# Performance work log

Measured on AMD Instinct MI355X. Metric: run time of the kernel, lower is better.

The kernel has to match this reference:

```python
import jax, jax.numpy as jnp
import numpy as np

D_MODEL = 1024
NUM_HEADS = 16
HEAD_DIM = D_MODEL // NUM_HEADS
BATCH, SEQ = 4, 4096


def setup_inputs() -> dict:
    key = jax.random.key(0)
    ks = jax.random.split(key, 12)
    std = 0.02
    inp = {
        "query": jax.random.normal(ks[0], (BATCH, SEQ, D_MODEL), dtype=jnp.float32),
        "key": jax.random.normal(ks[1], (BATCH, SEQ, D_MODEL), dtype=jnp.float32),
        "value": jax.random.normal(ks[2], (BATCH, SEQ, D_MODEL), dtype=jnp.float32),
        "mask": jax.random.randint(ks[3], (BATCH, SEQ, 1, 1), 0, 2, dtype=jnp.int32),
        "Wq": jax.random.normal(ks[4], (D_MODEL, D_MODEL), dtype=jnp.float32) * std,
        "bq": jnp.zeros((D_MODEL,), dtype=jnp.float32),
        "Wk": jax.random.normal(ks[5], (D_MODEL, D_MODEL), dtype=jnp.float32) * std,
        "bk": jnp.zeros((D_MODEL,), dtype=jnp.float32),
        "Wv": jax.random.normal(ks[6], (D_MODEL, D_MODEL), dtype=jnp.float32) * std,
        "bv": jnp.zeros((D_MODEL,), dtype=jnp.float32),
        "Wo": jax.random.normal(ks[7], (D_MODEL, D_MODEL), dtype=jnp.float32) * std,
        "bo": jnp.zeros((D_MODEL,), dtype=jnp.float32),
    }
    return inp


def reference(query, key, value, mask, Wq, bq, Wk, bk, Wv, bv, Wo, bo):
    b = query.shape[0]
    # QKV projections (torch nn.Linear: x @ W.T + b)
    Q = query @ Wq.T + bq
    K = key @ Wk.T + bk
    V = value @ Wv.T + bv
    # [b, s, H, hd] -> [b, H, s, hd]
    Q = Q.reshape(b, -1, NUM_HEADS, HEAD_DIM).transpose(0, 2, 1, 3)
    K = K.reshape(b, -1, NUM_HEADS, HEAD_DIM).transpose(0, 2, 1, 3)
    V = V.reshape(b, -1, NUM_HEADS, HEAD_DIM).transpose(0, 2, 1, 3)
    # NOTE: faithful to the original's mislabeled einsum: tensors are [b,H,s,hd]
    # but labels treat axis1 as 'q' and axis2 as 'h', so energy is
    # [batch, seq, heads_q, heads_k] and softmax mixes over heads.
    energy = jnp.einsum('nqhd,nkhd->nhqk', Q, K)
    energy = jnp.where(mask == 0, jnp.float32(-1e20), energy)
    attention = jax.nn.softmax(energy / jnp.sqrt(jnp.float32(D_MODEL)), axis=3)
    # output labeled nqhd -> [b, heads, seq, hd]
    x = jnp.einsum('nhql,nlhd->nqhd', attention, V)
    x = x.transpose(0, 2, 1, 3).reshape(b, -1, D_MODEL)  # [b, s, d_model]
    return x @ Wo.T + bo
```

## Files before the change

kernel.cpp:

```cpp
#include <hip/hip_runtime.h>


typedef unsigned int u32;
typedef unsigned short u16;
typedef __attribute__((ext_vector_type(4))) float f32x4;
typedef __attribute__((ext_vector_type(8))) short bf16x8;

__device__ __forceinline__ void async_copy16(const void* g, void* l) {
  __builtin_amdgcn_global_load_lds(
      (const __attribute__((address_space(1))) void*)g,
      (__attribute__((address_space(3))) void*)l, 16, 0, 0);
}

__device__ __forceinline__ u32 pk_bf16(float a, float b) {
  u32 ua = (__builtin_bit_cast(u32, a) + 0x8000u) >> 16;
  u32 ub = (__builtin_bit_cast(u32, b) + 0x8000u) & 0xFFFF0000u;
  return ua | ub;
}
__device__ __forceinline__ float bflo(u32 u) { return __builtin_bit_cast(float, u << 16); }
__device__ __forceinline__ float bfhi(u32 u) { return __builtin_bit_cast(float, u & 0xFFFF0000u); }

struct F8 { float f[8]; };
__device__ __forceinline__ F8 unp8(uint4 u) {
  F8 r;
  r.f[0] = bflo(u.x); r.f[1] = bfhi(u.x);
  r.f[2] = bflo(u.y); r.f[3] = bfhi(u.y);
  r.f[4] = bflo(u.z); r.f[5] = bfhi(u.z);
  r.f[6] = bflo(u.w); r.f[7] = bfhi(u.w);
  return r;
}

__global__ void cvt_w4(const float* __restrict__ s0, const float* __restrict__ s1,
                       const float* __restrict__ s2, const float* __restrict__ s3,
                       u16* __restrict__ dst) {
  int z = blockIdx.y;
  const float* s = (z == 0) ? s0 : (z == 1) ? s1 : (z == 2) ? s2 : s3;
  u16* d = dst + (size_t)z * (1024 * 1024);
  int i = (blockIdx.x * 256 + threadIdx.x) * 4;
  float4 f = *(const float4*)(s + i);
  uint2 u;
  u.x = pk_bf16(f.x, f.y);
  u.y = pk_bf16(f.z, f.w);
  *(uint2*)(d + i) = u;
}

__global__ void cvt_in3(const float* __restrict__ s0, const float* __restrict__ s1,
                        const float* __restrict__ s2, u16* __restrict__ dst) {
  int z = blockIdx.y;
  const float* s = (z == 0) ? s0 : (z == 1) ? s1 : s2;
  u16* d = dst + (size_t)z * 16777216;
  int i = (blockIdx.x * 256 + threadIdx.x) * 4;
  float4 f = *(const float4*)(s + i);
  uint2 u;
  u.x = pk_bf16(f.x, f.y);
  u.y = pk_bf16(f.z, f.w);
  *(uint2*)(d + i) = u;
}

template <bool AF32, bool OUTBF>
__device__ __forceinline__ void gemm_tile(const void* __restrict__ Ap,
                                          const u16* __restrict__ Bp,
                                          const float* __restrict__ bias,
                                          void* __restrict__ Cp,
                                          int m0, int n0, u16* As, u16* Bs) {
  constexpr int KD = 1024;
  constexpr int ND = 1024;
  const int t = threadIdx.x;
  const int lane = t & 63, w = t >> 6;
  const int wr = (w >> 1) * 64, wc = (w & 1) * 64;
  const int lr = lane & 15, quad = lane >> 4;
  f32x4 acc[4][4] = {};

  for (int k0 = 0; k0 < KD; k0 += 32) {
    __syncthreads();
#pragma unroll
    for (int i = 0; i < 2; i++) {
      int c = i * 256 + t;
      int r = c >> 2, c8 = (c & 3) * 8;
      async_copy16(Bp + ((size_t)(n0 + r) * KD + k0 + c8), &Bs[c * 8]);
    }
    if constexpr (AF32) {
      const float* Af = (const float*)Ap;
      const int r = t >> 2, c8 = (t & 3) * 8;
      const float4* s0 = (const float4*)(Af + (size_t)(m0 + r) * KD + k0 + c8);
      const float4* s1 = (const float4*)(Af + (size_t)(m0 + 64 + r) * KD + k0 + c8);
      float4 f0 = s0[0], f1 = s0[1];
      float4 f2 = s1[0], f3 = s1[1];
      uint4 u0 = { pk_bf16(f0.x, f0.y), pk_bf16(f0.z, f0.w),
                   pk_bf16(f1.x, f1.y), pk_bf16(f1.z, f1.w) };
      uint4 u1 = { pk_bf16(f2.x, f2.y), pk_bf16(f2.z, f2.w),
                   pk_bf16(f3.x, f3.y), pk_bf16(f3.z, f3.w) };
      *(uint4*)&As[t * 8] = u0;
      *(uint4*)&As[(256 + t) * 8] = u1;
    } else {
      const u16* Ab = (const u16*)Ap;
#pragma unroll
      for (int i = 0; i < 2; i++) {
        int c = i * 256 + t;
        int r = c >> 2, c8 = (c & 3) * 8;
        async_copy16(Ab + ((size_t)(m0 + r) * KD + k0 + c8), &As[c * 8]);
      }
    }
    __syncthreads();

    bf16x8 af[4], bfr[4];
#pragma unroll
    for (int mi = 0; mi < 4; mi++)
      af[mi] = *(const bf16x8*)&As[(wr + mi * 16 + lr) * 32 + quad * 8];
#pragma unroll
    for (int ni = 0; ni < 4; ni++)
      bfr[ni] = *(const bf16x8*)&Bs[(wc + ni * 16 + lr) * 32 + quad * 8];
#pragma unroll
    for (int mi = 0; mi < 4; mi++)
#pragma unroll
      for (int ni = 0; ni < 4; ni++)
        acc[mi][ni] = __builtin_amdgcn_mfma_f32_16x16x32_bf16(af[mi], bfr[ni], acc[mi][ni], 0, 0, 0);
  }

#pragma unroll
  for (int ni = 0; ni < 4; ni++) {
    int col = n0 + wc + ni * 16 + lr;
    float bv = bias[col];
#pragma unroll
    for (int mi = 0; mi < 4; mi++) {
      int row = m0 + wr + mi * 16 + quad * 4;
#pragma unroll
      for (int r = 0; r < 4; r++) {
        float val = acc[mi][ni][r] + bv;
        if constexpr (OUTBF) {
          ((u16*)Cp)[(size_t)(row + r) * ND + col] =
              (u16)((__builtin_bit_cast(u32, val) + 0x8000u) >> 16);
        } else {
          ((float*)Cp)[(size_t)(row + r) * ND + col] = val;
        }
      }
    }
  }
}

template <bool AF32>
__global__ __launch_bounds__(256) void gemm_qkv(
    const void* __restrict__ a0, const void* __restrict__ a1, const void* __restrict__ a2,
    const u16* __restrict__ W, const float* __restrict__ b0, const float* __restrict__ b1,
    const float* __restrict__ b2, u16* __restrict__ out) {
  __shared__ alignas(16) u16 As[128 * 32];
  __shared__ alignas(16) u16 Bs[128 * 32];
  const int lin = blockIdx.x;
  const int c = lin & 7;
  const int i = lin >> 3;
  const int z = i >> 7;
  const int r = i & 127;
  const int m = c * 16 + (r >> 3);
  const int n = r & 7;
  const void* A = (z == 0) ? a0 : (z == 1) ? a1 : a2;
  const float* bias = (z == 0) ? b0 : (z == 1) ? b1 : b2;
  gemm_tile<AF32, true>(A, W + (size_t)z * 1048576, bias, out + (size_t)z * 16777216,
                        m * 128, n * 128, As, Bs);
}

__global__ __launch_bounds__(256) void gemm_o(
    const u16* __restrict__ X, const u16* __restrict__ W,
    const float* __restrict__ bias, float* __restrict__ C) {
  __shared__ alignas(16) u16 As[128 * 32];
  __shared__ alignas(16) u16 Bs[128 * 32];
  const int lin = blockIdx.x;
  const int c = lin & 7;
  const int i = lin >> 3;
  const int m = c * 16 + (i >> 3);
  const int n = i & 7;
  gemm_tile<false, false>(X, W, bias, C, m * 128, n * 128, As, Bs);
}

__global__ __launch_bounds__(256) void attn_mix(
    const u16* __restrict__ Q, const u16* __restrict__ K,
    const u16* __restrict__ V, const int* __restrict__ mask,
    u16* __restrict__ X) {
  constexpr int RS = 72;
  __shared__ alignas(16) u16 qs[4][16 * RS];
  __shared__ alignas(16) u16 ks[4][16 * RS];
  __shared__ alignas(16) u16 vs[4][16 * RS];

  const int w = threadIdx.x >> 6;
  const int lane = threadIdx.x & 63;
  const int p = blockIdx.x * 4 + w;
  const size_t base = (size_t)p * 1024;

  {
    const uint4* Qg = (const uint4*)(Q + base);
    const uint4* Kg = (const uint4*)(K + base);
    const uint4* Vg = (const uint4*)(V + base);
#pragma unroll
    for (int h = 0; h < 2; h++) {
      int j = h * 64 + lane;
      int off = (j >> 3) * RS + (j & 7) * 8;
      *(uint4*)&qs[w][off] = Qg[j];
      *(uint4*)&ks[w][off] = Kg[j];
      *(uint4*)&vs[w][off] = Vg[j];
    }
  }
  const int mk = mask[p];

  const int qh = lane >> 2, g = lane & 3;
  float e0 = 0.f, e1 = 0.f, e2 = 0.f, e3 = 0.f;
  {
    const u16* qr = &qs[w][qh * RS];
    const u16* k0r = &ks[w][(g * 4 + 0) * RS];
    const u16* k1r = &ks[w][(g * 4 + 1) * RS];
    const u16* k2r = &ks[w][(g * 4 + 2) * RS];
    const u16* k3r = &ks[w][(g * 4 + 3) * RS];
#pragma unroll
    for (int c = 0; c < 8; c++) {
      F8 qf = unp8(*(const uint4*)&qr[c * 8]);
      F8 ka = unp8(*(const uint4*)&k0r[c * 8]);
      F8 kb = unp8(*(const uint4*)&k1r[c * 8]);
      F8 kc = unp8(*(const uint4*)&k2r[c * 8]);
      F8 kd = unp8(*(const uint4*)&k3r[c * 8]);
#pragma unroll
      for (int j = 0; j < 8; j++) {
        e0 += qf.f[j] * ka.f[j];
        e1 += qf.f[j] * kb.f[j];
        e2 += qf.f[j] * kc.f[j];
        e3 += qf.f[j] * kd.f[j];
      }
    }
  }
  const float sc = mk ? 0.03125f : 0.0f;
  float v0 = e0 * sc, v1 = e1 * sc, v2 = e2 * sc, v3 = e3 * sc;
  float mx = fmaxf(fmaxf(v0, v1), fmaxf(v2, v3));
  mx = fmaxf(mx, __shfl_xor(mx, 1, 64));
  mx = fmaxf(mx, __shfl_xor(mx, 2, 64));
  float p0 = __expf(v0 - mx), p1 = __expf(v1 - mx), p2 = __expf(v2 - mx), p3 = __expf(v3 - mx);
  float s = p0 + p1 + p2 + p3;
  s += __shfl_xor(s, 1, 64);
  s += __shfl_xor(s, 2, 64);
  float inv = 1.0f / s;
  float a0 = p0 * inv, a1 = p1 * inv, a2 = p2 * inv, a3 = p3 * inv;

  float xa[16];
#pragma unroll
  for (int i = 0; i < 16; i++) xa[i] = 0.f;
#pragma unroll
  for (int g2 = 0; g2 < 4; g2++) {
    int src = (lane & ~3) | g2;
    float w0 = __shfl(a0, src, 64);
    float w1 = __shfl(a1, src, 64);
    float w2 = __shfl(a2, src, 64);
    float w3 = __shfl(a3, src, 64);
    const float wv[4] = { w0, w1, w2, w3 };
#pragma unroll
    for (int j4 = 0; j4 < 4; j4++) {
      int kh = g2 * 4 + j4;
      float wgt = wv[j4];
      F8 va = unp8(*(const uint4*)&vs[w][kh * RS + g * 16]);
      F8 vb = unp8(*(const uint4*)&vs[w][kh * RS + g * 16 + 8]);
#pragma unroll
      for (int j = 0; j < 8; j++) {
        xa[j] += wgt * va.f[j];
        xa[8 + j] += wgt * vb.f[j];
      }
    }
  }
  uint4 o0 = { pk_bf16(xa[0], xa[1]), pk_bf16(xa[2], xa[3]),
               pk_bf16(xa[4], xa[5]), pk_bf16(xa[6], xa[7]) };
  uint4 o1 = { pk_bf16(xa[8], xa[9]), pk_bf16(xa[10], xa[11]),
               pk_bf16(xa[12], xa[13]), pk_bf16(xa[14], xa[15]) };
  uint4* Xp = (uint4*)(X + base);
  Xp[lane * 2] = o0;
  Xp[lane * 2 + 1] = o1;
}

extern "C" void kernel_launch(void* const* d_in, const int* in_sizes, int n_in,
                              void* d_out, int out_size, void* d_ws, size_t ws_size,
                              hipStream_t stream) {
  const float* q    = (const float*)d_in[0];
  const float* k    = (const float*)d_in[1];
  const float* v    = (const float*)d_in[2];
  const int*   mask = (const int*)d_in[3];
  const float* Wq   = (const float*)d_in[4];
  const float* bq   = (const float*)d_in[5];
  const float* Wk   = (const float*)d_in[6];
  const float* bk   = (const float*)d_in[7];
  const float* Wv   = (const float*)d_in[8];
  const float* bv   = (const float*)d_in[9];
  const float* Wo   = (const float*)d_in[10];
  const float* bo   = (const float*)d_in[11];

  u16* wsb = (u16*)d_ws;
  const bool big = ws_size >= 209715200ull;

  if (big) {
    u16* Wqkv = wsb;
    u16* Wob  = wsb + 3145728;
    u16* qb   = wsb + 4194304;
    u16* Qb   = wsb + 54525952;
    u16* Kb   = Qb + 16777216;
    u16* Vb   = Kb + 16777216;
    u16* Xb   = qb;
    cvt_w4<<<dim3(1024, 4), 256, 0, stream>>>(Wq, Wk, Wv, Wo, wsb);
    cvt_in3<<<dim3(16384, 3), 256, 0, stream>>>(q, k, v, qb);
    gemm_qkv<false><<<3072, 256, 0, stream>>>(qb, qb + 16777216, qb + 33554432,
                                              Wqkv, bq, bk, bv, Qb);
    attn_mix<<<4096, 256, 0, stream>>>(Qb, Kb, Vb, mask, Xb);
    gemm_o<<<1024, 256, 0, stream>>>(Xb, Wob, bo, (float*)d_out);
  } else {
    u16* Wqkv = wsb;
    u16* Wob  = wsb + 3145728;
    u16* Qb   = wsb + 4194304;
    u16* Kb   = Qb + 16777216;
    u16* Vb   = Kb + 16777216;
    u16* Xb   = Vb + 16777216;
    cvt_w4<<<dim3(1024, 4), 256, 0, stream>>>(Wq, Wk, Wv, Wo, wsb);
    gemm_qkv<true><<<3072, 256, 0, stream>>>(q, k, v, Wqkv, bq, bk, bv, Qb);
    attn_mix<<<4096, 256, 0, stream>>>(Qb, Kb, Vb, mask, Xb);
    gemm_o<<<1024, 256, 0, stream>>>(Xb, Wob, bo, (float*)d_out);
  }
}
```

Measured before the change: 460.1 us.

## Replace 128x128 GEMMs with 256x256 8-wave pipelined bf16 MFMA kernel

```diff
diff --git a/kernel.cpp b/kernel.cpp
--- a/kernel.cpp
+++ b/kernel.cpp
@@ -55,6 +55,188 @@
   u.x = pk_bf16(f.x, f.y);
   u.y = pk_bf16(f.z, f.w);
   *(uint2*)(d + i) = u;
+}
+
+
+#define BAR() asm volatile("s_barrier" ::: "memory")
+#define VMC(n) asm volatile("s_waitcnt vmcnt(" #n ")" ::: "memory")
+
+template <bool OUTBF>
+__device__ __forceinline__ void gemm256_8p(
+    const u16* __restrict__ A, const u16* __restrict__ Bm,
+    const float* __restrict__ bias, void* __restrict__ Cp,
+    int gm0, int gn0, u16* sm) {
+  const int tid = threadIdx.x;
+  const int lane = tid & 63;
+  const int w = tid >> 6;
+  const int wm = w >> 2, wn = w & 3;
+  const int wr0 = wm * 128, wc0 = wn * 64;
+  const int lr = lane & 15, quad = lane >> 4;
+
+  const int sr = tid >> 3;
+  const int sc = tid & 7;
+
+  f32x4 acc[8][4];
+#pragma unroll
+  for (int i = 0; i < 8; i++)
+#pragma unroll
+    for (int j = 0; j < 4; j++) acc[i][j] = (f32x4){0.f, 0.f, 0.f, 0.f};
+
+  bf16x8 aA[4][2];
+  bf16x8 bB[4][2];
+
+#define STAGE_A(buf, h, T) do {                                              \
+    int k0_ = ((T) & 15) * 64;                                               \
+    u16* lb_ = sm + (buf) * 16384;                                           \
+    _Pragma("unroll")                                                        \
+    for (int ld_ = 0; ld_ < 2; ld_++) {                                      \
+      int row_ = ld_ * 128 + (h) * 64 + sr;       \
+      int cs_ = (sc ^ (row_ & 7)) * 8;              \
+      async_copy16(A + (size_t)(gm0 + row_) * 1024 + k0_ + cs_,              \
+                   lb_ + row_ * 64 + sc * 8);                                \
+    }                                                                        \
+  } while (0)
+
+#define STAGE_B(buf, bh, T) do {                                             \
+    int k0_ = ((T) & 15) * 64;                                               \
+    u16* lb_ = sm + 32768 + (buf) * 16384;                                   \
+    _Pragma("unroll")                                                        \
+    for (int ld_ = 0; ld_ < 2; ld_++) {                                      \
+      int ri_ = ld_ * 64 + sr;                                               \
+      int row_ = ((ri_ >> 5) << 6) + (bh) * 32 + (ri_ & 31);                 \
+      int cs_ = (sc ^ (row_ & 7)) * 8;                                       \
+      async_copy16(Bm + (size_t)(gn0 + row_) * 1024 + k0_ + cs_,             \
+                   lb_ + row_ * 64 + sc * 8);                                \
+    }                                                                        \
+  } while (0)
+
+#define READ_A(mh, buf) do {                                                 \
+    const u16* lb_ = sm + (buf) * 16384;                                     \
+    _Pragma("unroll")                                                        \
+    for (int m4_ = 0; m4_ < 4; m4_++)                                        \
+      _Pragma("unroll")                                                      \
+      for (int kk_ = 0; kk_ < 2; kk_++) {                                    \
+        int row_ = wr0 + ((mh) * 4 + m4_) * 16 + lr;                         \
+        aA[m4_][kk_] = *(const bf16x8*)(lb_ + row_ * 64 +                    \
+                         (((kk_ * 4 + quad) ^ (row_ & 7)) * 8));             \
+      }                                                                      \
+  } while (0)
+
+#define READ_B(nh, buf) do {                                                 \
+    const u16* lb_ = sm + 32768 + (buf) * 16384;                             \
+    _Pragma("unroll")                                                        \
+    for (int n2_ = 0; n2_ < 2; n2_++)                                        \
+      _Pragma("unroll")                                                      \
+      for (int kk_ = 0; kk_ < 2; kk_++) {                                    \
+        int row_ = wc0 + ((nh) * 2 + n2_) * 16 + lr;                         \
+        bB[(nh) * 2 + n2_][kk_] = *(const bf16x8*)(lb_ + row_ * 64 +         \
+                         (((kk_ * 4 + quad) ^ (row_ & 7)) * 8));             \
+      }                                                                      \
+  } while (0)
+
+#define MFMA16(mh, nh) do {                                                  \
+    __builtin_amdgcn_s_setprio(1);                                           \
+    _Pragma("unroll")                                                        \
+    for (int m4_ = 0; m4_ < 4; m4_++)                                        \
+      _Pragma("unroll")                                                      \
+      for (int n2_ = 0; n2_ < 2; n2_++)                                      \
+        _Pragma("unroll")                                                    \
+        for (int kk_ = 0; kk_ < 2; kk_++)                                    \
+          acc[(mh) * 4 + m4_][(nh) * 2 + n2_] =                              \
+              __builtin_amdgcn_mfma_f32_16x16x32_bf16(                       \
+                  aA[m4_][kk_], bB[(nh) * 2 + n2_][kk_],                     \
+                  acc[(mh) * 4 + m4_][(nh) * 2 + n2_], 0, 0, 0);             \
+    __builtin_amdgcn_s_setprio(0);                                           \
+  } while (0)
+
+  STAGE_A(0, 0, 0); STAGE_B(0, 0, 0); STAGE_A(0, 1, 0); STAGE_B(0, 1, 0);
+  VMC(4);
+  STAGE_A(1, 0, 1); STAGE_B(1, 0, 1); STAGE_A(1, 1, 1);
+  VMC(6);
+  BAR();
+
+  for (int i = 0; i < 8; i++) {
+    const int T1 = 2 * i + 1, T2 = 2 * i + 2, T3 = 2 * i + 3;
+    READ_A(0, 0); READ_B(0, 0);
+    STAGE_B(1, 1, T1);
+    BAR(); MFMA16(0, 0); BAR();
+    READ_B(1, 0);
+    STAGE_A(0, 0, T2);
+    BAR(); MFMA16(0, 1); BAR();
+    READ_A(1, 0);
+    STAGE_B(0, 0, T2);
+    BAR(); MFMA16(1, 0); BAR();
+    STAGE_A(0, 1, T2);
+    VMC(6);
+    BAR(); MFMA16(1, 1); BAR();
+    READ_A(0, 1); READ_B(0, 1);
+    STAGE_B(0, 1, T2);
+    BAR(); MFMA16(0, 0); BAR();
+    READ_B(1, 1);
+    STAGE_A(1, 0, T3);
+    BAR(); MFMA16(0, 1); BAR();
+    READ_A(1, 1);
+    STAGE_B(1, 0, T3);
+    BAR(); MFMA16(1, 0); BAR();
+    STAGE_A(1, 1, T3);
+    VMC(6);
+    BAR(); MFMA16(1, 1); BAR();
+  }
+  VMC(0);
+
+#pragma unroll
+  for (int ni = 0; ni < 4; ni++) {
+    int col = gn0 + wc0 + ni * 16 + lr;
+    float bv = bias[col];
+#pragma unroll
+    for (int mi = 0; mi < 8; mi++) {
+      int row = gm0 + wr0 + mi * 16 + quad * 4;
+#pragma unroll
+      for (int r = 0; r < 4; r++) {
+        float val = acc[mi][ni][r] + bv;
+        if constexpr (OUTBF) {
+          ((u16*)Cp)[(size_t)(row + r) * 1024 + col] =
+              (u16)((__builtin_bit_cast(u32, val) + 0x8000u) >> 16);
+        } else {
+          ((float*)Cp)[(size_t)(row + r) * 1024 + col] = val;
+        }
+      }
+    }
+  }
+#undef STAGE_A
+#undef STAGE_B
+#undef READ_A
+#undef READ_B
+#undef MFMA16
+}
+
+__global__ __launch_bounds__(512, 2) void gemm_qkv8(
+    const u16* __restrict__ X, const u16* __restrict__ W,
+    const float* __restrict__ b0, const float* __restrict__ b1,
+    const float* __restrict__ b2, u16* __restrict__ out) {
+  __shared__ alignas(16) u16 sm[65536];
+  const int lin = blockIdx.x;
+  const int c = lin & 7;
+  const int i = lin >> 3;
+  const int z = i >> 5;
+  const int r = i & 31;
+  const int m = c * 8 + (r >> 2);
+  const int n = r & 3;
+  const float* bias = (z == 0) ? b0 : (z == 1) ? b1 : b2;
+  gemm256_8p<true>(X + (size_t)z * 16777216, W + (size_t)z * 1048576, bias,
+                   out + (size_t)z * 16777216, m * 256, n * 256, sm);
+}
+
+__global__ __launch_bounds__(512, 2) void gemm_o8(
+    const u16* __restrict__ X, const u16* __restrict__ W,
+    const float* __restrict__ bias, float* __restrict__ C) {
+  __shared__ alignas(16) u16 sm[65536];
+  const int lin = blockIdx.x;
+  const int c = lin & 7;
+  const int i = lin >> 3;
+  const int m = c * 8 + (i >> 2);
+  const int n = i & 3;
+  gemm256_8p<false>(X, W, bias, C, m * 256, n * 256, sm);
 }
 
 template <bool AF32, bool OUTBF>
@@ -158,19 +340,6 @@
                         m * 128, n * 128, As, Bs);
 }
 
-__global__ __launch_bounds__(256) void gemm_o(
-    const u16* __restrict__ X, const u16* __restrict__ W,
-    const float* __restrict__ bias, float* __restrict__ C) {
-  __shared__ alignas(16) u16 As[128 * 32];
-  __shared__ alignas(16) u16 Bs[128 * 32];
-  const int lin = blockIdx.x;
-  const int c = lin & 7;
-  const int i = lin >> 3;
-  const int m = c * 16 + (i >> 3);
-  const int n = i & 7;
-  gemm_tile<false, false>(X, W, bias, C, m * 128, n * 128, As, Bs);
-}
-
 __global__ __launch_bounds__(256) void attn_mix(
     const u16* __restrict__ Q, const u16* __restrict__ K,
     const u16* __restrict__ V, const int* __restrict__ mask,
@@ -298,10 +467,9 @@
     u16* Xb   = qb;
     cvt_w4<<<dim3(1024, 4), 256, 0, stream>>>(Wq, Wk, Wv, Wo, wsb);
     cvt_in3<<<dim3(16384, 3), 256, 0, stream>>>(q, k, v, qb);
-    gemm_qkv<false><<<3072, 256, 0, stream>>>(qb, qb + 16777216, qb + 33554432,
-                                              Wqkv, bq, bk, bv, Qb);
+    gemm_qkv8<<<768, 512, 0, stream>>>(qb, Wqkv, bq, bk, bv, Qb);
     attn_mix<<<4096, 256, 0, stream>>>(Qb, Kb, Vb, mask, Xb);
-    gemm_o<<<1024, 256, 0, stream>>>(Xb, Wob, bo, (float*)d_out);
+    gemm_o8<<<256, 512, 0, stream>>>(Xb, Wob, bo, (float*)d_out);
   } else {
     u16* Wqkv = wsb;
     u16* Wob  = wsb + 3145728;
@@ -312,6 +480,6 @@
     cvt_w4<<<dim3(1024, 4), 256, 0, stream>>>(Wq, Wk, Wv, Wo, wsb);
     gemm_qkv<true><<<3072, 256, 0, stream>>>(q, k, v, Wqkv, bq, bk, bv, Qb);
     attn_mix<<<4096, 256, 0, stream>>>(Qb, Kb, Vb, mask, Xb);
-    gemm_o<<<1024, 256, 0, stream>>>(Xb, Wob, bo, (float*)d_out);
-  }
-}
+    gemm_o8<<<256, 512, 0, stream>>>(Xb, Wob, bo, (float*)d_out);
+  }
+}
```

Measured after the change: 432.5 us. -6.0%, faster.
